# Performance work log

Measured on AMD Instinct MI355X. Metric: run time of the kernel, lower is better.

The kernel has to match this reference:

```python
import jax, jax.numpy as jnp
import numpy as np

B, S, D = 4, 2048, 1024
H = 2 * D          # hidden_dim = 2*n_embd
A = H // 16        # adapt_dim
E = 8              # num_experts
GS = 4             # group_size
G = E // GS        # num_groups
K = 2              # top-k experts within group


def _ln(x, g, b, eps=1e-5):
    m = x.mean(-1, keepdims=True)
    v = ((x - m) ** 2).mean(-1, keepdims=True)
    return (x - m) * jax.lax.rsqrt(v + eps) * g + b


def setup_inputs() -> dict:
    key = jax.random.key(0)
    ks = jax.random.split(key, 14)
    n = lambda k, shape, s: jax.random.normal(k, shape, jnp.float32) * s
    sc = 1.0 / float(np.sqrt(D))
    asc = 0.01 / float(np.sqrt(A))
    return {
        'x': n(ks[0], (B, S, D), 1.0),
        'Wu': n(ks[1], (H, D), sc),        # shared_up
        'Wg': n(ks[2], (H, D), sc),        # shared_gate
        'Wd': n(ks[3], (D, H), sc),        # shared_down
        'Wpre': n(ks[4], (A, D), sc * 0.01),   # pre_adapt
        'Wpost': n(ks[5], (A, H), sc * 0.01),  # post_adapt
        'ln_g': jnp.ones((A,), jnp.float32),
        'ln_b': jnp.zeros((A,), jnp.float32),
        'Wap': n(ks[6], (H, A), sc * 0.01),    # adapt_proj
        'Wea': n(ks[7], (E, A, A), asc),       # per-expert adapter linears
        'ln_eg': jnp.ones((E, A), jnp.float32),
        'ln_eb': jnp.zeros((E, A), jnp.float32),
        'Wep': n(ks[8], (H, A), asc),          # expert_proj
        'Wop': n(ks[9], (D, H), asc),          # output_proj
        'Wgr': n(ks[10], (G, D), 0.001),       # router_group
        'Wer': n(ks[11], (GS, D), 0.001),      # router_expert
    }


def _forward(x, Wu, Wg, Wd, Wpre, Wpost, ln_g, ln_b, Wap, Wea, ln_eg, ln_eb, Wep, Wop, Wgr, Wer):
    N = B * S
    xf = x.reshape(N, D)
    # --- hierarchical router ---
    gl = xf @ Wgr.T                              # [N,G]
    gp = jax.nn.softmax(gl, axis=-1)
    gw, gi = jax.lax.top_k(gp, 1)                # top-1 group
    el = xf @ Wer.T                              # [N,GS]
    ep = jax.nn.softmax(el, axis=-1)
    lw, li = jax.lax.top_k(ep, K)                # top-k local experts
    lw = lw / (lw.sum(-1, keepdims=True) + 1e-7)
    fw = gw * lw                                 # [N,K] final weights
    idx = gi * GS + li                           # [N,K] global expert ids (distinct per token)
    dispatch = jnp.zeros((N, E), x.dtype).at[jnp.arange(N)[:, None], idx].set(fw)
    load = dispatch.sum(0)
    target = load.sum() / E
    rloss = 0.001 * (jnp.mean((load - target) ** 2) + jnp.mean(gl ** 2) + jnp.mean(el ** 2))
    # --- shared expert MLP ---
    hidden = jax.nn.silu(x @ Wg.T) * (x @ Wu.T)  # [B,S,H]
    ai = _ln(x @ Wpre.T, ln_g, ln_b)             # [B,S,A]
    ao = _ln(hidden @ Wpost.T, ln_g, ln_b)       # [B,S,A]
    aw = jax.nn.silu(jnp.clip(jnp.einsum('bsa,bta->bst', ai, ao), -5.0, 5.0))  # [B,S,S]
    adapt = jnp.einsum('bst,bta->bsa', aw, ai) @ Wap.T
    hidden = hidden + 0.1 * adapt
    shared = hidden @ Wd.T                       # [B,S,D]
    # --- expert group (dense form of masked gather/scatter; w==0 off-mask) ---
    w = dispatch.reshape(B, S, E)
    h0 = x @ Wpre.T                              # [B,S,A]
    he = _ln(jnp.einsum('bsa,eca->bsec', h0, Wea), ln_eg, ln_eb)  # [B,S,E,A]
    M = Wop @ Wep                                # output_proj o expert_proj, [D,A]
    out = shared * w.sum(-1, keepdims=True) + 0.1 * jnp.einsum('bsec,bse,dc->bsd', he, w, M)
    return out, rloss


def reference(x, Wu, Wg, Wd, Wpre, Wpost, ln_g, ln_b, Wap, Wea, ln_eg, ln_eb, Wep, Wop, Wgr, Wer):
    return _forward(x, Wu, Wg, Wd, Wpre, Wpost, ln_g, ln_b, Wap, Wea, ln_eg, ln_eb, Wep, Wop, Wgr, Wer)
```

## Files before the change

kernel.cpp:

```cpp
#include <hip/hip_runtime.h>
#include <math.h>


typedef __bf16 bf16_t;
typedef __attribute__((ext_vector_type(8))) __bf16 bf16x8;
typedef __attribute__((ext_vector_type(4))) float f32x4;

__device__ __forceinline__ float b2f(bf16_t v) { return (float)v; }
__device__ __forceinline__ bf16_t f2b(float v) { return (bf16_t)v; }
__device__ __forceinline__ float siluf(float v) { return v / (1.f + expf(-v)); }

static constexpr int Bb = 4, S = 2048, D = 1024, H = 2048, A = 128, E = 8;
static constexpr int N = Bb * S;

typedef __attribute__((address_space(1))) void gvoid;
typedef __attribute__((address_space(3))) void svoid;
__device__ __forceinline__ void gll16(const bf16_t* g, bf16_t* l) {
  __builtin_amdgcn_global_load_lds((gvoid*)g, (svoid*)l, 16, 0, 0);
}

__device__ __forceinline__ long tidx(int row, int k, int K, int lgTR) {
  int TRm = (1 << lgTR) - 1;
  int q = (k >> 3) & 3;
  int p = q ^ ((row >> 1) & 3);
  return ((((long)(row >> lgTR) * (K >> 5) + (k >> 5)) << lgTR) + (row & TRm)) * 32 +
         ((long)p << 3);
}

__device__ __forceinline__ bf16x8 ld8f(const float* p) {
  float4 a = *reinterpret_cast<const float4*>(p);
  float4 b = *reinterpret_cast<const float4*>(p + 4);
  bf16x8 r;
  r[0] = f2b(a.x); r[1] = f2b(a.y); r[2] = f2b(a.z); r[3] = f2b(a.w);
  r[4] = f2b(b.x); r[5] = f2b(b.y); r[6] = f2b(b.z); r[7] = f2b(b.w);
  return r;
}
__device__ __forceinline__ void split8(const float* p, bf16x8& h, bf16x8& l) {
  float4 a = *reinterpret_cast<const float4*>(p);
  float4 b = *reinterpret_cast<const float4*>(p + 4);
  float v[8] = {a.x, a.y, a.z, a.w, b.x, b.y, b.z, b.w};
#pragma unroll
  for (int j = 0; j < 8; j++) {
    bf16_t hh = f2b(v[j]);
    h[j] = hh;
    l[j] = f2b(v[j] - b2f(hh));
  }
}
__device__ __forceinline__ bf16x8 ld8m(const void* p, int row, int k, int K, int m) {
  if (m == 1) return ld8f(reinterpret_cast<const float*>(p) + (long)row * K + k);
  if (m == 2)
    return *reinterpret_cast<const bf16x8*>(
        reinterpret_cast<const bf16_t*>(p) + tidx(row, k, K, 7));
  return *reinterpret_cast<const bf16x8*>(
      reinterpret_cast<const bf16_t*>(p) + (long)row * K + k);
}

template <int LGTR, int LGNKS>
__global__ __launch_bounds__(256) void split_tiled(
    const float* __restrict__ in, bf16_t* __restrict__ hi,
    bf16_t* __restrict__ lo, long total, int K) {
  long stride = (long)gridDim.x * 256;
  for (long o = (long)blockIdx.x * 256 + threadIdx.x; o < total; o += stride) {
    int p = (int)(o & 3);
    long t = o >> 2;
    int r = (int)(t & ((1 << LGTR) - 1));
    long t2 = t >> LGTR;
    int ks = (int)(t2 & ((1 << LGNKS) - 1));
    long rt = t2 >> LGNKS;
    long row = (rt << LGTR) + r;
    int k = (ks << 5) + ((p ^ ((r >> 1) & 3)) << 3);
    bf16x8 h, l;
    split8(in + row * K + k, h, l);
    reinterpret_cast<bf16x8*>(hi)[o] = h;
    reinterpret_cast<bf16x8*>(lo)[o] = l;
  }
}

template <int LGTR, int LGNKS>
__global__ __launch_bounds__(256) void split_tiled2(
    const float* __restrict__ s0, bf16_t* __restrict__ h0, bf16_t* __restrict__ l0,
    const float* __restrict__ s1, bf16_t* __restrict__ h1, bf16_t* __restrict__ l1,
    long total, int K) {
  const float* in = blockIdx.z ? s1 : s0;
  bf16_t* hi = blockIdx.z ? h1 : h0;
  bf16_t* lo = blockIdx.z ? l1 : l0;
  long stride = (long)gridDim.x * 256;
  for (long o = (long)blockIdx.x * 256 + threadIdx.x; o < total; o += stride) {
    int p = (int)(o & 3);
    long t = o >> 2;
    int r = (int)(t & ((1 << LGTR) - 1));
    long t2 = t >> LGTR;
    int ks = (int)(t2 & ((1 << LGNKS) - 1));
    long rt = t2 >> LGNKS;
    long row = (rt << LGTR) + r;
    int k = (ks << 5) + ((p ^ ((r >> 1) & 3)) << 3);
    bf16x8 h, l;
    split8(in + row * K + k, h, l);
    reinterpret_cast<bf16x8*>(hi)[o] = h;
    reinterpret_cast<bf16x8*>(lo)[o] = l;
  }
}

template <int WM, int WN, int MODE>
__global__ __launch_bounds__(256) void gemm_nt_b(
    const void* __restrict__ Ag, const void* __restrict__ Bg,
    void* __restrict__ Cv, int M, int Nn, int K,
    const float* __restrict__ aux, int aF, int bF) {
  constexpr int BM = 2 * WM, BN = 2 * WN, AM = WM / 16, AN = WN / 16;
  constexpr int LDT = 40;
  __shared__ alignas(16) bf16_t As[BM * LDT];
  __shared__ alignas(16) bf16_t Bs[BN * LDT];

  const int tid = threadIdx.x;
  const int wave = tid >> 6, lane = tid & 63;
  const int wr = wave >> 1, wc = wave & 1;
  const int quad = lane >> 4, l16 = lane & 15;
  const int rowA0 = blockIdx.y * BM, rowB0 = blockIdx.x * BN;

  f32x4 acc[AM][AN] = {};

  for (int k0 = 0; k0 < K; k0 += 32) {
    for (int c = tid; c < BM * 4; c += 256) {
      int r = c >> 2, kc = c & 3;
      *reinterpret_cast<bf16x8*>(&As[r * LDT + kc * 8]) =
          ld8m(Ag, rowA0 + r, k0 + kc * 8, K, aF);
    }
    for (int c = tid; c < BN * 4; c += 256) {
      int r = c >> 2, kc = c & 3;
      *reinterpret_cast<bf16x8*>(&Bs[r * LDT + kc * 8]) =
          ld8m(Bg, rowB0 + r, k0 + kc * 8, K, bF);
    }
    __syncthreads();
    bf16x8 af[AM], bfv[AN];
#pragma unroll
    for (int i = 0; i < AM; i++)
      af[i] = *reinterpret_cast<bf16x8*>(&As[(wr * WM + i * 16 + l16) * LDT + quad * 8]);
#pragma unroll
    for (int j = 0; j < AN; j++)
      bfv[j] = *reinterpret_cast<bf16x8*>(&Bs[(wc * WN + j * 16 + l16) * LDT + quad * 8]);
#pragma unroll
    for (int i = 0; i < AM; i++)
#pragma unroll
      for (int j = 0; j < AN; j++)
        acc[i][j] = __builtin_amdgcn_mfma_f32_16x16x32_bf16(af[i], bfv[j], acc[i][j], 0, 0, 0);
    __syncthreads();
  }

#pragma unroll
  for (int i = 0; i < AM; i++)
#pragma unroll
    for (int j = 0; j < AN; j++)
#pragma unroll
      for (int r = 0; r < 4; r++) {
        int row = rowA0 + wr * WM + i * 16 + quad * 4 + r;
        int col = rowB0 + wc * WN + j * 16 + l16;
        long o = (long)row * Nn + col;
        float v = acc[i][j][r];
        if constexpr (MODE == 0) {
          reinterpret_cast<bf16_t*>(Cv)[o] = f2b(v);
        } else if constexpr (MODE == 1) {
          v = fminf(fmaxf(v, -5.f), 5.f);
          reinterpret_cast<bf16_t*>(Cv)[o] = f2b(siluf(v));
        } else if constexpr (MODE == 2) {
          float* C = reinterpret_cast<float*>(Cv);
          C[o] = C[o] + 0.1f * v;
        } else {
          float* C = reinterpret_cast<float*>(Cv);
          C[o] = C[o] * aux[row] + 0.1f * v;
        }
      }
}

__global__ __launch_bounds__(256) void gemm_gu_g(
    const bf16_t* __restrict__ xhT, const bf16_t* __restrict__ xlT,
    const bf16_t* __restrict__ WghT, const bf16_t* __restrict__ WglT,
    const bf16_t* __restrict__ WuhT, const bf16_t* __restrict__ WulT,
    bf16_t* __restrict__ Hh, bf16_t* __restrict__ Hl) {
  __shared__ alignas(16) bf16_t Ah[128 * 32];
  __shared__ alignas(16) bf16_t Al[128 * 32];
  __shared__ alignas(16) bf16_t B1h[64 * 32];
  __shared__ alignas(16) bf16_t B1l[64 * 32];
  __shared__ alignas(16) bf16_t B2h[64 * 32];
  __shared__ alignas(16) bf16_t B2l[64 * 32];

  const int tid = threadIdx.x;
  const int wave = tid >> 6, lane = tid & 63;
  const int wr = wave >> 1, wc = wave & 1;
  const int quad = lane >> 4, l16 = lane & 15;
  const int sw = (quad ^ ((l16 >> 1) & 3)) << 3;
  const int lid = blockIdx.y * gridDim.x + blockIdx.x;
  const int nper = (gridDim.x * gridDim.y) >> 3;
  const int nl = (lid & 7) * nper + (lid >> 3);
  const int bm = nl >> 5, bn = nl & 31;
  constexpr int nks = D / 32;
  const int wo = wave << 9;

  f32x4 ag[4][2] = {}, au[4][2] = {};

  for (int ks = 0; ks < nks; ks++) {
    long ao = (((long)bm * nks + ks) << 12) + wo + lane * 8;
    long bo = (((long)bn * nks + ks) << 11) + wo + lane * 8;
    gll16(xhT + ao, Ah + wo);
    gll16(xhT + ao + 2048, Ah + wo + 2048);
    gll16(xlT + ao, Al + wo);
    gll16(xlT + ao + 2048, Al + wo + 2048);
    gll16(WghT + bo, B1h + wo);
    gll16(WglT + bo, B1l + wo);
    gll16(WuhT + bo, B2h + wo);
    gll16(WulT + bo, B2l + wo);
    __syncthreads();
    bf16x8 afh[4], afl[4], b1h[2], b1l[2], b2h[2], b2l[2];
#pragma unroll
    for (int i = 0; i < 4; i++) {
      int ro = (wr * 64 + i * 16 + l16) * 32 + sw;
      afh[i] = *reinterpret_cast<bf16x8*>(&Ah[ro]);
      afl[i] = *reinterpret_cast<bf16x8*>(&Al[ro]);
    }
#pragma unroll
    for (int j = 0; j < 2; j++) {
      int ro = (wc * 32 + j * 16 + l16) * 32 + sw;
      b1h[j] = *reinterpret_cast<bf16x8*>(&B1h[ro]);
      b1l[j] = *reinterpret_cast<bf16x8*>(&B1l[ro]);
      b2h[j] = *reinterpret_cast<bf16x8*>(&B2h[ro]);
      b2l[j] = *reinterpret_cast<bf16x8*>(&B2l[ro]);
    }
#pragma unroll
    for (int i = 0; i < 4; i++)
#pragma unroll
      for (int j = 0; j < 2; j++) {
        ag[i][j] = __builtin_amdgcn_mfma_f32_16x16x32_bf16(afh[i], b1h[j], ag[i][j], 0, 0, 0);
        ag[i][j] = __builtin_amdgcn_mfma_f32_16x16x32_bf16(afh[i], b1l[j], ag[i][j], 0, 0, 0);
        ag[i][j] = __builtin_amdgcn_mfma_f32_16x16x32_bf16(afl[i], b1h[j], ag[i][j], 0, 0, 0);
        au[i][j] = __builtin_amdgcn_mfma_f32_16x16x32_bf16(afh[i], b2h[j], au[i][j], 0, 0, 0);
        au[i][j] = __builtin_amdgcn_mfma_f32_16x16x32_bf16(afh[i], b2l[j], au[i][j], 0, 0, 0);
        au[i][j] = __builtin_amdgcn_mfma_f32_16x16x32_bf16(afl[i], b2h[j], au[i][j], 0, 0, 0);
      }
    __syncthreads();
  }

#pragma unroll
  for (int i = 0; i < 4; i++)
#pragma unroll
    for (int j = 0; j < 2; j++)
#pragma unroll
      for (int r = 0; r < 4; r++) {
        int row = bm * 128 + wr * 64 + i * 16 + quad * 4 + r;
        int col = bn * 64 + wc * 32 + j * 16 + l16;
        long o = tidx(row, col, H, 7) + (col & 7);
        float v = siluf(ag[i][j][r]) * au[i][j][r];
        bf16_t hh = f2b(v);
        Hh[o] = hh;
        Hl[o] = f2b(v - b2f(hh));
      }
}

__global__ __launch_bounds__(256) void gemm_dn_g(
    const bf16_t* __restrict__ HhT, const bf16_t* __restrict__ HlT,
    const bf16_t* __restrict__ WdhT, const bf16_t* __restrict__ WdlT,
    const bf16_t* __restrict__ hw2, const bf16_t* __restrict__ Mb2,
    const float* __restrict__ wsum, float* __restrict__ Cg) {
  __shared__ alignas(16) bf16_t Ah[128 * 32];
  __shared__ alignas(16) bf16_t Al[128 * 32];
  __shared__ alignas(16) bf16_t Bh[128 * 32];
  __shared__ alignas(16) bf16_t Bl[128 * 32];

  const int tid = threadIdx.x;
  const int wave = tid >> 6, lane = tid & 63;
  const int wr = wave >> 1, wc = wave & 1;
  const int quad = lane >> 4, l16 = lane & 15;
  const int sw = (quad ^ ((l16 >> 1) & 3)) << 3;
  const int lid = blockIdx.y * gridDim.x + blockIdx.x;
  const int nper = (gridDim.x * gridDim.y) >> 3;
  const int nl = (lid & 7) * nper + (lid >> 3);
  const int by = nl >> 3, bx = nl & 7;
  constexpr int nks = H / 32;
  const int wo = wave << 9;

  f32x4 acc[4][4] = {};

  for (int ks = 0; ks < nks; ks++) {
    long ao = (((long)by * nks + ks) << 12) + wo + lane * 8;
    long bo = (((long)bx * nks + ks) << 12) + wo + lane * 8;
    gll16(HhT + ao, Ah + wo);
    gll16(HhT + ao + 2048, Ah + wo + 2048);
    gll16(HlT + ao, Al + wo);
    gll16(HlT + ao + 2048, Al + wo + 2048);
    gll16(WdhT + bo, Bh + wo);
    gll16(WdhT + bo + 2048, Bh + wo + 2048);
    gll16(WdlT + bo, Bl + wo);
    gll16(WdlT + bo + 2048, Bl + wo + 2048);
    __syncthreads();
    bf16x8 afh[4], afl[4], bfh[4], bfl[4];
#pragma unroll
    for (int i = 0; i < 4; i++) {
      int ro = (wr * 64 + i * 16 + l16) * 32 + sw;
      afh[i] = *reinterpret_cast<bf16x8*>(&Ah[ro]);
      afl[i] = *reinterpret_cast<bf16x8*>(&Al[ro]);
    }
#pragma unroll
    for (int j = 0; j < 4; j++) {
      int ro = (wc * 64 + j * 16 + l16) * 32 + sw;
      bfh[j] = *reinterpret_cast<bf16x8*>(&Bh[ro]);
      bfl[j] = *reinterpret_cast<bf16x8*>(&Bl[ro]);
    }
#pragma unroll
    for (int i = 0; i < 4; i++)
#pragma unroll
      for (int j = 0; j < 4; j++) {
        acc[i][j] = __builtin_amdgcn_mfma_f32_16x16x32_bf16(afh[i], bfh[j], acc[i][j], 0, 0, 0);
        acc[i][j] = __builtin_amdgcn_mfma_f32_16x16x32_bf16(afh[i], bfl[j], acc[i][j], 0, 0, 0);
        acc[i][j] = __builtin_amdgcn_mfma_f32_16x16x32_bf16(afl[i], bfh[j], acc[i][j], 0, 0, 0);
      }
    __syncthreads();
  }

  {
    const int rrow = wave * 16 + (lane >> 2);
    const int pp = lane & 3;
    for (int ck = 0; ck < 8; ck++) {
      int r0 = rrow, r1 = rrow + 64;
      int q0 = (pp ^ ((r0 >> 1) & 3)) << 3;
      int q1 = (pp ^ ((r1 >> 1) & 3)) << 3;
      gll16(hw2 + ((long)(by * 128 + r0) * 256 + ck * 32 + q0), Ah + wo);
      gll16(hw2 + ((long)(by * 128 + r1) * 256 + ck * 32 + q1), Ah + wo + 2048);
      gll16(Mb2 + ((long)(bx * 128 + r0) * 256 + ck * 32 + q0), Bh + wo);
      gll16(Mb2 + ((long)(bx * 128 + r1) * 256 + ck * 32 + q1), Bh + wo + 2048);
      __syncthreads();
      bf16x8 af2[4], bf2[4];
#pragma unroll
      for (int i = 0; i < 4; i++)
        af2[i] = *reinterpret_cast<bf16x8*>(&Ah[(wr * 64 + i * 16 + l16) * 32 + sw]);
#pragma unroll
      for (int j = 0; j < 4; j++)
        bf2[j] = *reinterpret_cast<bf16x8*>(&Bh[(wc * 64 + j * 16 + l16) * 32 + sw]);
#pragma unroll
      for (int i = 0; i < 4; i++)
#pragma unroll
        for (int j = 0; j < 4; j++)
          acc[i][j] = __builtin_amdgcn_mfma_f32_16x16x32_bf16(af2[i], bf2[j], acc[i][j], 0, 0, 0);
      __syncthreads();
    }
  }

#pragma unroll
  for (int i = 0; i < 4; i++)
#pragma unroll
    for (int j = 0; j < 4; j++)
#pragma unroll
      for (int r = 0; r < 4; r++) {
        int row = by * 128 + wr * 64 + i * 16 + quad * 4 + r;
        int col = bx * 128 + wc * 64 + j * 16 + l16;
        Cg[(long)row * D + col] = wsum[row] * acc[i][j][r];
      }
}

__global__ __launch_bounds__(256) void fused_adapt(
    const bf16_t* __restrict__ aib, const bf16_t* __restrict__ aob,
    const bf16_t* __restrict__ aiT, bf16_t* __restrict__ outp,
    int oLd, int oOff, float cscale) {
  constexpr int LDQ = 136;
  constexpr int LDP = 72;
  __shared__ alignas(16) bf16_t Qs[64 * LDQ];
  __shared__ alignas(16) bf16_t Os[64 * LDQ];
  __shared__ alignas(16) bf16_t Ps[64 * LDP];
  __shared__ alignas(16) bf16_t Vs[128 * LDP];

  const int tid = threadIdx.x;
  const int wave = tid >> 6, lane = tid & 63;
  const int wr = wave >> 1, wc = wave & 1;
  const int quad = lane >> 4, l16 = lane & 15;
  const int b = blockIdx.y;
  const int q0 = blockIdx.x * 64;

  for (int c = tid; c < 1024; c += 256) {
    int r = c >> 4, cc = c & 15;
    *reinterpret_cast<bf16x8*>(&Qs[r * LDQ + cc * 8]) =
        *reinterpret_cast<const bf16x8*>(&aib[((long)b * S + q0 + r) * A + cc * 8]);
  }

  f32x4 o[2][4] = {};

  for (int tt = 0; tt < S / 64; tt++) {
    const int t0 = tt * 64;
    __syncthreads();
    for (int c = tid; c < 1024; c += 256) {
      int r = c >> 4, cc = c & 15;
      *reinterpret_cast<bf16x8*>(&Os[r * LDQ + cc * 8]) =
          *reinterpret_cast<const bf16x8*>(&aob[((long)b * S + t0 + r) * A + cc * 8]);
    }
    for (int c = tid; c < 1024; c += 256) {
      int r = c >> 3, cc = c & 7;
      *reinterpret_cast<bf16x8*>(&Vs[r * LDP + cc * 8]) =
          *reinterpret_cast<const bf16x8*>(&aiT[((long)b * A + r) * S + t0 + cc * 8]);
    }
    __syncthreads();
    f32x4 p[2][2] = {};
#pragma unroll
    for (int ks = 0; ks < 4; ks++) {
      bf16x8 af[2], bfv[2];
#pragma unroll
      for (int i = 0; i < 2; i++)
        af[i] = *reinterpret_cast<bf16x8*>(&Qs[(wr * 32 + i * 16 + l16) * LDQ + ks * 32 + quad * 8]);
#pragma unroll
      for (int j = 0; j < 2; j++)
        bfv[j] = *reinterpret_cast<bf16x8*>(&Os[(wc * 32 + j * 16 + l16) * LDQ + ks * 32 + quad * 8]);
#pragma unroll
      for (int i = 0; i < 2; i++)
#pragma unroll
        for (int j = 0; j < 2; j++)
          p[i][j] = __builtin_amdgcn_mfma_f32_16x16x32_bf16(af[i], bfv[j], p[i][j], 0, 0, 0);
    }
#pragma unroll
    for (int i = 0; i < 2; i++)
#pragma unroll
      for (int j = 0; j < 2; j++)
#pragma unroll
        for (int r = 0; r < 4; r++) {
          int row = wr * 32 + i * 16 + quad * 4 + r;
          int col = wc * 32 + j * 16 + l16;
          float v = fminf(fmaxf(p[i][j][r], -5.f), 5.f);
          Ps[row * LDP + col] = f2b(siluf(v));
        }
    __syncthreads();
#pragma unroll
    for (int ks = 0; ks < 2; ks++) {
      bf16x8 paf[2], vbf[4];
#pragma unroll
      for (int i = 0; i < 2; i++)
        paf[i] = *reinterpret_cast<bf16x8*>(&Ps[(wr * 32 + i * 16 + l16) * LDP + ks * 32 + quad * 8]);
#pragma unroll
      for (int j = 0; j < 4; j++)
        vbf[j] = *reinterpret_cast<bf16x8*>(&Vs[(wc * 64 + j * 16 + l16) * LDP + ks * 32 + quad * 8]);
#pragma unroll
      for (int i = 0; i < 2; i++)
#pragma unroll
        for (int j = 0; j < 4; j++)
          o[i][j] = __builtin_amdgcn_mfma_f32_16x16x32_bf16(paf[i], vbf[j], o[i][j], 0, 0, 0);
    }
  }

#pragma unroll
  for (int i = 0; i < 2; i++)
#pragma unroll
    for (int j = 0; j < 4; j++)
#pragma unroll
      for (int r = 0; r < 4; r++) {
        int row = q0 + wr * 32 + i * 16 + quad * 4 + r;
        int col = wc * 64 + j * 16 + l16;
        long token = (long)b * S + row;
        outp[token * oLd + oOff + col] = f2b(o[i][j][r] * cscale);
      }
}

__global__ __launch_bounds__(256) void gemm_mb_splitk(
    const float* __restrict__ Ag, const bf16_t* __restrict__ Bg,
    float* __restrict__ Mp, int M, int Nn, int K) {
  constexpr int BM = 64, BN = 64, LDT = 40;
  __shared__ alignas(16) bf16_t As[BM * LDT];
  __shared__ alignas(16) bf16_t Bs[BN * LDT];
  const int tid = threadIdx.x;
  const int wave = tid >> 6, lane = tid & 63;
  const int wr = wave >> 1, wc = wave & 1;
  const int quad = lane >> 4, l16 = lane & 15;
  const int rowA0 = blockIdx.y * BM, rowB0 = blockIdx.x * BN;
  const int kz = blockIdx.z;
  const int ks0 = kz * (K / 8), ks1 = ks0 + K / 8;

  f32x4 acc[2][2] = {};
  for (int k0 = ks0; k0 < ks1; k0 += 32) {
    for (int c = tid; c < BM * 4; c += 256) {
      int r = c >> 2, kc = c & 3;
      *reinterpret_cast<bf16x8*>(&As[r * LDT + kc * 8]) =
          ld8f(Ag + (long)(rowA0 + r) * K + k0 + kc * 8);
    }
    for (int c = tid; c < BN * 4; c += 256) {
      int r = c >> 2, kc = c & 3;
      *reinterpret_cast<bf16x8*>(&Bs[r * LDT + kc * 8]) =
          *reinterpret_cast<const bf16x8*>(&Bg[(long)(rowB0 + r) * K + k0 + kc * 8]);
    }
    __syncthreads();
    bf16x8 af[2], bfv[2];
#pragma unroll
    for (int i = 0; i < 2; i++)
      af[i] = *reinterpret_cast<bf16x8*>(&As[(wr * 32 + i * 16 + l16) * LDT + quad * 8]);
#pragma unroll
    for (int j = 0; j < 2; j++)
      bfv[j] = *reinterpret_cast<bf16x8*>(&Bs[(wc * 32 + j * 16 + l16) * LDT + quad * 8]);
#pragma unroll
    for (int i = 0; i < 2; i++)
#pragma unroll
      for (int j = 0; j < 2; j++)
        acc[i][j] = __builtin_amdgcn_mfma_f32_16x16x32_bf16(af[i], bfv[j], acc[i][j], 0, 0, 0);
    __syncthreads();
  }
#pragma unroll
  for (int i = 0; i < 2; i++)
#pragma unroll
    for (int j = 0; j < 2; j++)
#pragma unroll
      for (int r = 0; r < 4; r++) {
        int row = rowA0 + wr * 32 + i * 16 + quad * 4 + r;
        int col = rowB0 + wc * 32 + j * 16 + l16;
        Mp[(long)kz * M * Nn + (long)row * Nn + col] = acc[i][j][r];
      }
}

__global__ __launch_bounds__(256) void mb_combine(
    const float* __restrict__ Mp, bf16_t* __restrict__ outp, int total,
    int ld, int coff) {
  int i = blockIdx.x * 256 + threadIdx.x;
  if (i >= total) return;
  float s = 0.f;
#pragma unroll
  for (int z = 0; z < 8; z++) s += Mp[(long)z * total + i];
  outp[(long)(i >> 7) * ld + coff + (i & 127)] = f2b(s);
}

__global__ __launch_bounds__(256) void gemm_dn_hl(
    const float* __restrict__ Ag, const float* __restrict__ Bg,
    float* __restrict__ Cg, int M, int Nn, int K) {
  constexpr int BM = 128, BN = 128, LDT = 40;
  __shared__ alignas(16) bf16_t Ah[BM * LDT];
  __shared__ alignas(16) bf16_t Al[BM * LDT];
  __shared__ alignas(16) bf16_t Bh[BN * LDT];
  __shared__ alignas(16) bf16_t Bl[BN * LDT];

  const int tid = threadIdx.x;
  const int wave = tid >> 6, lane = tid & 63;
  const int wr = wave >> 1, wc = wave & 1;
  const int quad = lane >> 4, l16 = lane & 15;
  const int rowA0 = blockIdx.y * BM, rowB0 = blockIdx.x * BN;

  f32x4 acc[4][4] = {};

  for (int k0 = 0; k0 < K; k0 += 32) {
    for (int c = tid; c < BM * 4; c += 256) {
      int r = c >> 2, kc = c & 3;
      bf16x8 h, l;
      split8(&Ag[(long)(rowA0 + r) * K + k0 + kc * 8], h, l);
      *reinterpret_cast<bf16x8*>(&Ah[r * LDT + kc * 8]) = h;
      *reinterpret_cast<bf16x8*>(&Al[r * LDT + kc * 8]) = l;
    }
    for (int c = tid; c < BN * 4; c += 256) {
      int r = c >> 2, kc = c & 3;
      bf16x8 h, l;
      split8(&Bg[(long)(rowB0 + r) * K + k0 + kc * 8], h, l);
      *reinterpret_cast<bf16x8*>(&Bh[r * LDT + kc * 8]) = h;
      *reinterpret_cast<bf16x8*>(&Bl[r * LDT + kc * 8]) = l;
    }
    __syncthreads();
    bf16x8 afh[4], afl[4], bfh[4], bfl[4];
#pragma unroll
    for (int i = 0; i < 4; i++) {
      int ro = (wr * 64 + i * 16 + l16) * LDT + quad * 8;
      afh[i] = *reinterpret_cast<bf16x8*>(&Ah[ro]);
      afl[i] = *reinterpret_cast<bf16x8*>(&Al[ro]);
    }
#pragma unroll
    for (int j = 0; j < 4; j++) {
      int ro = (wc * 64 + j * 16 + l16) * LDT + quad * 8;
      bfh[j] = *reinterpret_cast<bf16x8*>(&Bh[ro]);
      bfl[j] = *reinterpret_cast<bf16x8*>(&Bl[ro]);
    }
#pragma unroll
    for (int i = 0; i < 4; i++)
#pragma unroll
      for (int j = 0; j < 4; j++) {
        acc[i][j] = __builtin_amdgcn_mfma_f32_16x16x32_bf16(afh[i], bfh[j], acc[i][j], 0, 0, 0);
        acc[i][j] = __builtin_amdgcn_mfma_f32_16x16x32_bf16(afh[i], bfl[j], acc[i][j], 0, 0, 0);
        acc[i][j] = __builtin_amdgcn_mfma_f32_16x16x32_bf16(afl[i], bfh[j], acc[i][j], 0, 0, 0);
      }
    __syncthreads();
  }

#pragma unroll
  for (int i = 0; i < 4; i++)
#pragma unroll
    for (int j = 0; j < 4; j++)
#pragma unroll
      for (int r = 0; r < 4; r++) {
        int row = rowA0 + wr * 64 + i * 16 + quad * 4 + r;
        int col = rowB0 + wc * 64 + j * 16 + l16;
        Cg[(long)row * Nn + col] = acc[i][j][r];
      }
}

__global__ __launch_bounds__(256) void gemm_gu_hl(
    const float* __restrict__ x, const float* __restrict__ Wg,
    const float* __restrict__ Wu, float* __restrict__ Cg, int M, int Nn, int K) {
  constexpr int BM = 128, BN = 64, LDT = 40;
  __shared__ alignas(16) bf16_t Ah[BM * LDT];
  __shared__ alignas(16) bf16_t Al[BM * LDT];
  __shared__ alignas(16) bf16_t B1h[BN * LDT];
  __shared__ alignas(16) bf16_t B1l[BN * LDT];
  __shared__ alignas(16) bf16_t B2h[BN * LDT];
  __shared__ alignas(16) bf16_t B2l[BN * LDT];

  const int tid = threadIdx.x;
  const int wave = tid >> 6, lane = tid & 63;
  const int wr = wave >> 1, wc = wave & 1;
  const int quad = lane >> 4, l16 = lane & 15;
  const int rowA0 = blockIdx.y * BM, rowB0 = blockIdx.x * BN;

  f32x4 ag[4][2] = {}, au[4][2] = {};

  for (int k0 = 0; k0 < K; k0 += 32) {
    for (int c = tid; c < BM * 4; c += 256) {
      int r = c >> 2, kc = c & 3;
      bf16x8 h, l;
      split8(&x[(long)(rowA0 + r) * K + k0 + kc * 8], h, l);
      *reinterpret_cast<bf16x8*>(&Ah[r * LDT + kc * 8]) = h;
      *reinterpret_cast<bf16x8*>(&Al[r * LDT + kc * 8]) = l;
    }
    for (int c = tid; c < BN * 4; c += 256) {
      int r = c >> 2, kc = c & 3;
      long idx = (long)(rowB0 + r) * K + k0 + kc * 8;
      bf16x8 h, l;
      split8(&Wg[idx], h, l);
      *reinterpret_cast<bf16x8*>(&B1h[r * LDT + kc * 8]) = h;
      *reinterpret_cast<bf16x8*>(&B1l[r * LDT + kc * 8]) = l;
      split8(&Wu[idx], h, l);
      *reinterpret_cast<bf16x8*>(&B2h[r * LDT + kc * 8]) = h;
      *reinterpret_cast<bf16x8*>(&B2l[r * LDT + kc * 8]) = l;
    }
    __syncthreads();
    bf16x8 afh[4], afl[4], b1h[2], b1l[2], b2h[2], b2l[2];
#pragma unroll
    for (int i = 0; i < 4; i++) {
      int ro = (wr * 64 + i * 16 + l16) * LDT + quad * 8;
      afh[i] = *reinterpret_cast<bf16x8*>(&Ah[ro]);
      afl[i] = *reinterpret_cast<bf16x8*>(&Al[ro]);
    }
#pragma unroll
    for (int j = 0; j < 2; j++) {
      int ro = (wc * 32 + j * 16 + l16) * LDT + quad * 8;
      b1h[j] = *reinterpret_cast<bf16x8*>(&B1h[ro]);
      b1l[j] = *reinterpret_cast<bf16x8*>(&B1l[ro]);
      b2h[j] = *reinterpret_cast<bf16x8*>(&B2h[ro]);
      b2l[j] = *reinterpret_cast<bf16x8*>(&B2l[ro]);
    }
#pragma unroll
    for (int i = 0; i < 4; i++)
#pragma unroll
      for (int j = 0; j < 2; j++) {
        ag[i][j] = __builtin_amdgcn_mfma_f32_16x16x32_bf16(afh[i], b1h[j], ag[i][j], 0, 0, 0);
        ag[i][j] = __builtin_amdgcn_mfma_f32_16x16x32_bf16(afh[i], b1l[j], ag[i][j], 0, 0, 0);
        ag[i][j] = __builtin_amdgcn_mfma_f32_16x16x32_bf16(afl[i], b1h[j], ag[i][j], 0, 0, 0);
        au[i][j] = __builtin_amdgcn_mfma_f32_16x16x32_bf16(afh[i], b2h[j], au[i][j], 0, 0, 0);
        au[i][j] = __builtin_amdgcn_mfma_f32_16x16x32_bf16(afh[i], b2l[j], au[i][j], 0, 0, 0);
        au[i][j] = __builtin_amdgcn_mfma_f32_16x16x32_bf16(afl[i], b2h[j], au[i][j], 0, 0, 0);
      }
    __syncthreads();
  }

#pragma unroll
  for (int i = 0; i < 4; i++)
#pragma unroll
    for (int j = 0; j < 2; j++)
#pragma unroll
      for (int r = 0; r < 4; r++) {
        int row = rowA0 + wr * 64 + i * 16 + quad * 4 + r;
        int col = rowB0 + wc * 32 + j * 16 + l16;
        Cg[(long)row * Nn + col] = siluf(ag[i][j][r]) * au[i][j][r];
      }
}

__global__ __launch_bounds__(256) void router_kernel(
    const float* __restrict__ x, const float* __restrict__ Wgr,
    const float* __restrict__ Wer, int* __restrict__ eidx,
    float* __restrict__ fw, float* __restrict__ wsum,
    float* __restrict__ lpart) {
  __shared__ float part[4][12];
  const int wv = threadIdx.x >> 6;
  const int lane = threadIdx.x & 63;
  const int token = blockIdx.x * 4 + wv;
  if (lane < 12) part[wv][lane] = 0.f;
  const float* xp = x + (long)token * D;
  float xr[16];
#pragma unroll
  for (int i = 0; i < 16; i++) xr[i] = xp[lane + i * 64];
  float dots[6];
#pragma unroll
  for (int w = 0; w < 6; w++) {
    const float* wp = (w < 2) ? (Wgr + (long)w * D) : (Wer + (long)(w - 2) * D);
    float s = 0.f;
#pragma unroll
    for (int i = 0; i < 16; i++) s += xr[i] * wp[lane + i * 64];
#pragma unroll
    for (int off = 32; off; off >>= 1) s += __shfl_xor(s, off);
    dots[w] = s;
  }
  if (lane == 0) {
    float gl0 = dots[0], gl1 = dots[1];
    float mg = fmaxf(gl0, gl1);
    float e0 = expf(gl0 - mg), e1 = expf(gl1 - mg);
    float inv = 1.f / (e0 + e1);
    float gp0 = e0 * inv, gp1 = e1 * inv;
    int gi = (gp1 > gp0) ? 1 : 0;
    float gw = gi ? gp1 : gp0;
    float el[4] = {dots[2], dots[3], dots[4], dots[5]};
    float me = fmaxf(fmaxf(el[0], el[1]), fmaxf(el[2], el[3]));
    float ep[4], es = 0.f;
#pragma unroll
    for (int j = 0; j < 4; j++) { ep[j] = expf(el[j] - me); es += ep[j]; }
    float inve = 1.f / es;
#pragma unroll
    for (int j = 0; j < 4; j++) ep[j] *= inve;
    int i1 = 0;
    for (int j = 1; j < 4; j++) if (ep[j] > ep[i1]) i1 = j;
    int i2 = (i1 == 0) ? 1 : 0;
    for (int j = 0; j < 4; j++) if (j != i1 && j != i2 && ep[j] > ep[i2]) i2 = j;
    float l1 = ep[i1], l2 = ep[i2];
    float ils = 1.f / (l1 + l2 + 1e-7f);
    float f1 = gw * l1 * ils, f2 = gw * l2 * ils;
    eidx[token * 2] = gi * 4 + i1;
    eidx[token * 2 + 1] = gi * 4 + i2;
    fw[token * 2] = f1;
    fw[token * 2 + 1] = f2;
    wsum[token] = f1 + f2;
    part[wv][gi * 4 + i1] = f1;
    part[wv][gi * 4 + i2] = f2;
    part[wv][8] = gl0 * gl0 + gl1 * gl1;
    part[wv][9] = el[0] * el[0] + el[1] * el[1] + el[2] * el[2] + el[3] * el[3];
  }
  __syncthreads();
  if (threadIdx.x < 12) {
    lpart[(long)blockIdx.x * 12 + threadIdx.x] =
        part[0][threadIdx.x] + part[1][threadIdx.x] +
        part[2][threadIdx.x] + part[3][threadIdx.x];
  }
}

__global__ __launch_bounds__(256) void ln_rows(
    const bf16_t* __restrict__ in, const float* __restrict__ g,
    const float* __restrict__ b, bf16_t* __restrict__ out) {
  const int row = blockIdx.x * 4 + (threadIdx.x >> 6);
  const int lane = threadIdx.x & 63;
  const bf16_t* p = in + (long)row * A;
  float x0 = b2f(p[lane]), x1 = b2f(p[lane + 64]);
  float s = x0 + x1;
#pragma unroll
  for (int off = 32; off; off >>= 1) s += __shfl_xor(s, off);
  float mean = s * (1.f / 128.f);
  float d0 = x0 - mean, d1 = x1 - mean;
  float q = d0 * d0 + d1 * d1;
#pragma unroll
  for (int off = 32; off; off >>= 1) q += __shfl_xor(q, off);
  float r = rsqrtf(q * (1.f / 128.f) + 1e-5f);
  bf16_t* po = out + (long)row * A;
  po[lane] = f2b(d0 * r * g[lane] + b[lane]);
  po[lane + 64] = f2b(d1 * r * g[lane + 64] + b[lane + 64]);
}

__global__ __launch_bounds__(256) void transpose2d(
    const void* __restrict__ in, bf16_t* __restrict__ out, int R, int C, int isf) {
  __shared__ bf16_t t[32][33];
  const long zb = blockIdx.z;
  const long ib = zb * (long)R * C;
  bf16_t* op = out + zb * (long)R * C;
  const int r0 = blockIdx.y * 32, c0 = blockIdx.x * 32;
  const int tx = threadIdx.x & 31, ty = threadIdx.x >> 5;
#pragma unroll
  for (int i = 0; i < 4; i++) {
    long idx = ib + (long)(r0 + ty + i * 8) * C + c0 + tx;
    t[ty + i * 8][tx] = isf ? f2b(reinterpret_cast<const float*>(in)[idx])
                            : reinterpret_cast<const bf16_t*>(in)[idx];
  }
  __syncthreads();
#pragma unroll
  for (int i = 0; i < 4; i++) op[(long)(c0 + ty + i * 8) * R + r0 + tx] = t[tx][ty + i * 8];
}

__global__ __launch_bounds__(128) void expert_adapt(
    const bf16_t* __restrict__ h0, const bf16_t* __restrict__ WeaT,
    const float* __restrict__ ln_eg, const float* __restrict__ ln_eb,
    const int* __restrict__ eidx, const float* __restrict__ fw,
    bf16_t* __restrict__ hw, int ld, const float* __restrict__ wsc) {
  const int n = blockIdx.x;
  const int c = threadIdx.x;
  __shared__ float h0s[128];
  __shared__ float red[4];
  h0s[c] = b2f(h0[(long)n * A + c]);
  __syncthreads();
  float out = 0.f;
  for (int k = 0; k < 2; k++) {
    int e = eidx[n * 2 + k];
    e = min(max(e, 0), E - 1);
    float w = fw[n * 2 + k];
    const bf16_t* Wc = WeaT + (long)e * A * A + c;
    float t = 0.f;
#pragma unroll 8
    for (int a = 0; a < 128; a++) t += b2f(Wc[(long)a * A]) * h0s[a];
    float s = t, q = t * t;
#pragma unroll
    for (int off = 32; off; off >>= 1) { s += __shfl_xor(s, off); q += __shfl_xor(q, off); }
    if ((c & 63) == 0) { red[(c >> 6) * 2] = s; red[(c >> 6) * 2 + 1] = q; }
    __syncthreads();
    float Sx = red[0] + red[2], Qx = red[1] + red[3];
    float mean = Sx * (1.f / 128.f);
    float var = Qx * (1.f / 128.f) - mean * mean;
    float r = rsqrtf(var + 1e-5f);
    out += w * ((t - mean) * r * ln_eg[e * A + c] + ln_eb[e * A + c]);
    __syncthreads();
  }
  float sc = wsc ? (0.1f / wsc[n]) : 1.f;
  hw[(long)n * ld + c] = f2b(out * sc);
}

__global__ __launch_bounds__(256) void finalize_loss(
    const float* __restrict__ lpart, int nblk, float* __restrict__ outv) {
  float acc[10] = {};
  for (int b = threadIdx.x; b < nblk; b += 256) {
    const float* p = lpart + (long)b * 12;
#pragma unroll
    for (int c = 0; c < 10; c++) acc[c] += p[c];
  }
  __shared__ float red[10][4];
  const int lane = threadIdx.x & 63, wv = threadIdx.x >> 6;
#pragma unroll
  for (int c = 0; c < 10; c++) {
    float s = acc[c];
#pragma unroll
    for (int off = 32; off; off >>= 1) s += __shfl_xor(s, off);
    if (lane == 0) red[c][wv] = s;
  }
  __syncthreads();
  if (threadIdx.x == 0) {
    float loss[10];
#pragma unroll
    for (int c = 0; c < 10; c++)
      loss[c] = red[c][0] + red[c][1] + red[c][2] + red[c][3];
    float tl = 0.f;
    for (int e = 0; e < 8; e++) tl += loss[e];
    float target = tl / 8.f;
    float mse = 0.f;
    for (int e = 0; e < 8; e++) { float d = loss[e] - target; mse += d * d; }
    mse *= (1.f / 8.f);
    outv[0] = 0.001f * (mse + loss[8] / (float)(N * 2) + loss[9] / (float)(N * 4));
  }
}

extern "C" void kernel_launch(void* const* d_in, const int* in_sizes, int n_in,
                              void* d_out, int out_size, void* d_ws, size_t ws_size,
                              hipStream_t stream) {
  const float* x = (const float*)d_in[0];
  const float* Wu = (const float*)d_in[1];
  const float* Wg = (const float*)d_in[2];
  const float* Wd = (const float*)d_in[3];
  const float* Wpre = (const float*)d_in[4];
  const float* Wpost = (const float*)d_in[5];
  const float* ln_g = (const float*)d_in[6];
  const float* ln_b = (const float*)d_in[7];
  const float* Wap = (const float*)d_in[8];
  const float* Wea = (const float*)d_in[9];
  const float* ln_eg = (const float*)d_in[10];
  const float* ln_eb = (const float*)d_in[11];
  const float* Wep = (const float*)d_in[12];
  const float* Wop = (const float*)d_in[13];
  const float* Wgr = (const float*)d_in[14];
  const float* Wer = (const float*)d_in[15];
  float* out = (float*)d_out;

  char* ws = (char*)d_ws;
  size_t off = 0;
  auto alloc = [&](size_t bytes) { char* p = ws + off; off += (bytes + 255) & ~size_t(255); return p; };
  float* lpart = (float*)alloc((size_t)(N / 4) * 12 * 4);
  float* wsum = (float*)alloc((size_t)N * 4);
  float* fwb = (float*)alloc((size_t)N * 2 * 4);
  int* eidx = (int*)alloc((size_t)N * 2 * 4);
  bf16_t* Mb2 = (bf16_t*)alloc((size_t)D * 256 * 2);
  float* Mp = (float*)alloc((size_t)8 * D * A * 4);
  bf16_t* WepT = (bf16_t*)alloc((size_t)H * A * 2);
  bf16_t* WapT = (bf16_t*)alloc((size_t)H * A * 2);
  bf16_t* hw2 = (bf16_t*)alloc((size_t)N * 256 * 2);
  bf16_t* h0b = (bf16_t*)alloc((size_t)N * A * 2);
  bf16_t* aib = (bf16_t*)alloc((size_t)N * A * 2);
  bf16_t* scrA = (bf16_t*)alloc((size_t)N * A * 2);
  bf16_t* aob = (bf16_t*)alloc((size_t)N * A * 2);
  bf16_t* WeaT = (bf16_t*)alloc((size_t)E * A * A * 2);
  bf16_t* aopre = scrA;
  bf16_t* aiT = scrA;

  const bool big = ws_size >= ((size_t)140 << 20);
  float* hiddenF = nullptr;
  bf16_t *xh = nullptr, *xl = nullptr;
  bf16_t *Wgh = nullptr, *Wgl = nullptr, *Wuh = nullptr, *Wul = nullptr;
  bf16_t *Wdh = nullptr, *Wdl = nullptr, *Hh = nullptr, *Hl = nullptr;
  if (big) {
    xh = (bf16_t*)alloc((size_t)N * D * 2);
    xl = (bf16_t*)alloc((size_t)N * D * 2);
    Wgh = (bf16_t*)alloc((size_t)H * D * 2);
    Wgl = (bf16_t*)alloc((size_t)H * D * 2);
    Wuh = (bf16_t*)alloc((size_t)H * D * 2);
    Wul = (bf16_t*)alloc((size_t)H * D * 2);
    Wdh = (bf16_t*)alloc((size_t)D * H * 2);
    Wdl = (bf16_t*)alloc((size_t)D * H * 2);
    Hh = (bf16_t*)alloc((size_t)N * H * 2);
    Hl = (bf16_t*)alloc((size_t)N * H * 2);
  } else {
    hiddenF = (float*)alloc((size_t)N * H * 4);
  }
  (void)ws_size; (void)in_sizes; (void)n_in; (void)out_size;

  const dim3 blk(256);

  router_kernel<<<dim3(N / 4), blk, 0, stream>>>(x, Wgr, Wer, eidx, fwb, wsum, lpart);
  transpose2d<<<dim3(A / 32, A / 32, E), blk, 0, stream>>>(Wea, WeaT, A, A, 1);

  if (big) {
    split_tiled<7, 5><<<dim3(2048), blk, 0, stream>>>(x, xh, xl, (long)N * D / 8, D);
    split_tiled2<6, 5><<<dim3(512, 1, 2), blk, 0, stream>>>(
        Wg, Wgh, Wgl, Wu, Wuh, Wul, (long)H * D / 8, D);
    split_tiled<7, 6><<<dim3(512), blk, 0, stream>>>(Wd, Wdh, Wdl, (long)D * H / 8, H);
    gemm_gu_g<<<dim3(H / 64, N / 128), blk, 0, stream>>>(
        xh, xl, Wgh, Wgl, Wuh, Wul, Hh, Hl);
    gemm_nt_b<16, 32, 0><<<dim3(A / 64, N / 32), blk, 0, stream>>>(
        xh, Wpre, h0b, N, A, D, nullptr, 2, 1);
    ln_rows<<<dim3(N / 4), blk, 0, stream>>>(h0b, ln_g, ln_b, aib);
    gemm_nt_b<16, 32, 0><<<dim3(A / 64, N / 32), blk, 0, stream>>>(
        Hh, Wpost, aopre, N, A, H, nullptr, 2, 1);
    ln_rows<<<dim3(N / 4), blk, 0, stream>>>(aopre, ln_g, ln_b, aob);
    transpose2d<<<dim3(A / 32, S / 32, Bb), blk, 0, stream>>>(aib, aiT, S, A, 0);
    transpose2d<<<dim3(A / 32, H / 32, 1), blk, 0, stream>>>(Wep, WepT, H, A, 1);
    transpose2d<<<dim3(A / 32, H / 32, 1), blk, 0, stream>>>(Wap, WapT, H, A, 1);
    gemm_mb_splitk<<<dim3(A / 64, D / 64, 8), blk, 0, stream>>>(Wop, WepT, Mp, D, A, H);
    mb_combine<<<dim3((D * A + 255) / 256), blk, 0, stream>>>(Mp, Mb2, D * A, 256, 0);
    gemm_mb_splitk<<<dim3(A / 64, D / 64, 8), blk, 0, stream>>>(Wd, WapT, Mp, D, A, H);
    mb_combine<<<dim3((D * A + 255) / 256), blk, 0, stream>>>(Mp, Mb2, D * A, 256, 128);
    fused_adapt<<<dim3(S / 64, Bb), blk, 0, stream>>>(
        aib, aob, aiT, hw2, 256, 128, 0.1f);
    expert_adapt<<<dim3(N), dim3(128), 0, stream>>>(
        h0b, WeaT, ln_eg, ln_eb, eidx, fwb, hw2, 256, wsum);
    gemm_dn_g<<<dim3(D / 128, N / 128), blk, 0, stream>>>(
        Hh, Hl, Wdh, Wdl, hw2, Mb2, wsum, out);
  } else {
    bf16_t* adpreb = hw2 + (size_t)N * A;
    gemm_gu_hl<<<dim3(H / 64, N / 128), blk, 0, stream>>>(x, Wg, Wu, hiddenF, N, H, D);
    gemm_nt_b<16, 32, 0><<<dim3(A / 64, N / 32), blk, 0, stream>>>(
        x, Wpre, h0b, N, A, D, nullptr, 1, 1);
    ln_rows<<<dim3(N / 4), blk, 0, stream>>>(h0b, ln_g, ln_b, aib);
    gemm_nt_b<16, 32, 0><<<dim3(A / 64, N / 32), blk, 0, stream>>>(
        hiddenF, Wpost, aopre, N, A, H, nullptr, 1, 1);
    ln_rows<<<dim3(N / 4), blk, 0, stream>>>(aopre, ln_g, ln_b, aob);
    transpose2d<<<dim3(A / 32, S / 32, Bb), blk, 0, stream>>>(aib, aiT, S, A, 0);
    fused_adapt<<<dim3(S / 64, Bb), blk, 0, stream>>>(
        aib, aob, aiT, adpreb, 128, 0, 1.f);
    gemm_nt_b<64, 64, 2><<<dim3(H / 128, N / 128), blk, 0, stream>>>(
        adpreb, Wap, hiddenF, N, H, A, nullptr, 0, 1);
    gemm_dn_hl<<<dim3(D / 128, N / 128), blk, 0, stream>>>(hiddenF, Wd, out, N, D, H);
    transpose2d<<<dim3(A / 32, H / 32, 1), blk, 0, stream>>>(Wep, WepT, H, A, 1);
    gemm_mb_splitk<<<dim3(A / 64, D / 64, 8), blk, 0, stream>>>(Wop, WepT, Mp, D, A, H);
    mb_combine<<<dim3((D * A + 255) / 256), blk, 0, stream>>>(Mp, Mb2, D * A, 128, 0);
    expert_adapt<<<dim3(N), dim3(128), 0, stream>>>(
        h0b, WeaT, ln_eg, ln_eb, eidx, fwb, hw2, 128, nullptr);
    gemm_nt_b<64, 64, 3><<<dim3(D / 128, N / 128), blk, 0, stream>>>(
        hw2, Mb2, out, N, D, A, wsum, 0, 0);
  }

  finalize_loss<<<dim3(1), blk, 0, stream>>>(lpart, N / 4, out + (size_t)N * D);
}
```

Before: 731.5 us.

## Halve fused_adapt query tile, pre-convert adapter weights, merge weight transposes

fused_adapt now processes 32 query rows per block instead of 64, doubling the grid from 128 to 256 blocks so the device's compute units are better filled. Each block reloads the O/V tiles for fewer rows, so total load traffic goes up. Wpre and Wpost are converted to bf16 once by a new kernel, so the GEMMs no longer convert fp32 weights on the fly. The two weight transposes are merged into one launch.

```diff
diff --git a/kernel.cpp b/kernel.cpp
--- a/kernel.cpp
+++ b/kernel.cpp
@@ -101,6 +101,17 @@
   }
 }
 
+__global__ __launch_bounds__(256) void cvt_bf16_2(
+    const float* __restrict__ s0, bf16_t* __restrict__ d0, long n0,
+    const float* __restrict__ s1, bf16_t* __restrict__ d1, long n1) {
+  long total = n0 + n1;
+  long stride = (long)gridDim.x * 256;
+  for (long i = (long)blockIdx.x * 256 + threadIdx.x; i < total; i += stride) {
+    if (i < n0) reinterpret_cast<bf16x8*>(d0)[i] = ld8f(s0 + i * 8);
+    else reinterpret_cast<bf16x8*>(d1)[i - n0] = ld8f(s1 + (i - n0) * 8);
+  }
+}
+
 template <int WM, int WN, int MODE>
 __global__ __launch_bounds__(256) void gemm_nt_b(
     const void* __restrict__ Ag, const void* __restrict__ Bg,
@@ -360,9 +371,9 @@
     int oLd, int oOff, float cscale) {
   constexpr int LDQ = 136;
   constexpr int LDP = 72;
-  __shared__ alignas(16) bf16_t Qs[64 * LDQ];
+  __shared__ alignas(16) bf16_t Qs[32 * LDQ];
   __shared__ alignas(16) bf16_t Os[64 * LDQ];
-  __shared__ alignas(16) bf16_t Ps[64 * LDP];
+  __shared__ alignas(16) bf16_t Ps[32 * LDP];
   __shared__ alignas(16) bf16_t Vs[128 * LDP];
 
   const int tid = threadIdx.x;
@@ -370,15 +381,15 @@
   const int wr = wave >> 1, wc = wave & 1;
   const int quad = lane >> 4, l16 = lane & 15;
   const int b = blockIdx.y;
-  const int q0 = blockIdx.x * 64;
-
-  for (int c = tid; c < 1024; c += 256) {
+  const int q0 = blockIdx.x * 32;
+
+  for (int c = tid; c < 512; c += 256) {
     int r = c >> 4, cc = c & 15;
     *reinterpret_cast<bf16x8*>(&Qs[r * LDQ + cc * 8]) =
         *reinterpret_cast<const bf16x8*>(&aib[((long)b * S + q0 + r) * A + cc * 8]);
   }
 
-  f32x4 o[2][4] = {};
+  f32x4 o[4] = {};
 
   for (int tt = 0; tt < S / 64; tt++) {
     const int t0 = tt * 64;
@@ -394,62 +405,52 @@
           *reinterpret_cast<const bf16x8*>(&aiT[((long)b * A + r) * S + t0 + cc * 8]);
     }
     __syncthreads();
-    f32x4 p[2][2] = {};
+    f32x4 p[2] = {};
 #pragma unroll
     for (int ks = 0; ks < 4; ks++) {
-      bf16x8 af[2], bfv[2];
-#pragma unroll
-      for (int i = 0; i < 2; i++)
-        af[i] = *reinterpret_cast<bf16x8*>(&Qs[(wr * 32 + i * 16 + l16) * LDQ + ks * 32 + quad * 8]);
+      bf16x8 af =
+          *reinterpret_cast<bf16x8*>(&Qs[(wr * 16 + l16) * LDQ + ks * 32 + quad * 8]);
+      bf16x8 bfv[2];
 #pragma unroll
       for (int j = 0; j < 2; j++)
         bfv[j] = *reinterpret_cast<bf16x8*>(&Os[(wc * 32 + j * 16 + l16) * LDQ + ks * 32 + quad * 8]);
 #pragma unroll
-      for (int i = 0; i < 2; i++)
-#pragma unroll
-        for (int j = 0; j < 2; j++)
-          p[i][j] = __builtin_amdgcn_mfma_f32_16x16x32_bf16(af[i], bfv[j], p[i][j], 0, 0, 0);
-    }
-#pragma unroll
-    for (int i = 0; i < 2; i++)
-#pragma unroll
       for (int j = 0; j < 2; j++)
-#pragma unroll
-        for (int r = 0; r < 4; r++) {
-          int row = wr * 32 + i * 16 + quad * 4 + r;
-          int col = wc * 32 + j * 16 + l16;
-          float v = fminf(fmaxf(p[i][j][r], -5.f), 5.f);
-          Ps[row * LDP + col] = f2b(siluf(v));
-        }
+        p[j] = __builtin_amdgcn_mfma_f32_16x16x32_bf16(af, bfv[j], p[j], 0, 0, 0);
+    }
+#pragma unroll
+    for (int j = 0; j < 2; j++)
+#pragma unroll
+      for (int r = 0; r < 4; r++) {
+        int row = wr * 16 + quad * 4 + r;
+        int col = wc * 32 + j * 16 + l16;
+        float v = fminf(fmaxf(p[j][r], -5.f), 5.f);
+        Ps[row * LDP + col] = f2b(siluf(v));
+      }
     __syncthreads();
 #pragma unroll
     for (int ks = 0; ks < 2; ks++) {
-      bf16x8 paf[2], vbf[4];
-#pragma unroll
-      for (int i = 0; i < 2; i++)
-        paf[i] = *reinterpret_cast<bf16x8*>(&Ps[(wr * 32 + i * 16 + l16) * LDP + ks * 32 + quad * 8]);
+      bf16x8 paf =
+          *reinterpret_cast<bf16x8*>(&Ps[(wr * 16 + l16) * LDP + ks * 32 + quad * 8]);
+      bf16x8 vbf[4];
 #pragma unroll
       for (int j = 0; j < 4; j++)
         vbf[j] = *reinterpret_cast<bf16x8*>(&Vs[(wc * 64 + j * 16 + l16) * LDP + ks * 32 + quad * 8]);
 #pragma unroll
-      for (int i = 0; i < 2; i++)
-#pragma unroll
-        for (int j = 0; j < 4; j++)
-          o[i][j] = __builtin_amdgcn_mfma_f32_16x16x32_bf16(paf[i], vbf[j], o[i][j], 0, 0, 0);
-    }
-  }
-
-#pragma unroll
-  for (int i = 0; i < 2; i++)
-#pragma unroll
-    for (int j = 0; j < 4; j++)
-#pragma unroll
-      for (int r = 0; r < 4; r++) {
-        int row = q0 + wr * 32 + i * 16 + quad * 4 + r;
-        int col = wc * 64 + j * 16 + l16;
-        long token = (long)b * S + row;
-        outp[token * oLd + oOff + col] = f2b(o[i][j][r] * cscale);
-      }
+      for (int j = 0; j < 4; j++)
+        o[j] = __builtin_amdgcn_mfma_f32_16x16x32_bf16(paf, vbf[j], o[j], 0, 0, 0);
+    }
+  }
+
+#pragma unroll
+  for (int j = 0; j < 4; j++)
+#pragma unroll
+    for (int r = 0; r < 4; r++) {
+      int row = q0 + wr * 16 + quad * 4 + r;
+      int col = wc * 64 + j * 16 + l16;
+      long token = (long)b * S + row;
+      outp[token * oLd + oOff + col] = f2b(o[j][r] * cscale);
+    }
 }
 
 __global__ __launch_bounds__(256) void gemm_mb_splitk(
@@ -765,6 +766,24 @@
     long idx = ib + (long)(r0 + ty + i * 8) * C + c0 + tx;
     t[ty + i * 8][tx] = isf ? f2b(reinterpret_cast<const float*>(in)[idx])
                             : reinterpret_cast<const bf16_t*>(in)[idx];
+  }
+  __syncthreads();
+#pragma unroll
+  for (int i = 0; i < 4; i++) op[(long)(c0 + ty + i * 8) * R + r0 + tx] = t[tx][ty + i * 8];
+}
+
+__global__ __launch_bounds__(256) void transpose2d_pair(
+    const float* __restrict__ in0, bf16_t* __restrict__ out0,
+    const float* __restrict__ in1, bf16_t* __restrict__ out1, int R, int C) {
+  __shared__ bf16_t t[32][33];
+  const float* in = blockIdx.z ? in1 : in0;
+  bf16_t* op = blockIdx.z ? out1 : out0;
+  const int r0 = blockIdx.y * 32, c0 = blockIdx.x * 32;
+  const int tx = threadIdx.x & 31, ty = threadIdx.x >> 5;
+#pragma unroll
+  for (int i = 0; i < 4; i++) {
+    long idx = (long)(r0 + ty + i * 8) * C + c0 + tx;
+    t[ty + i * 8][tx] = f2b(in[idx]);
   }
   __syncthreads();
 #pragma unroll
@@ -872,6 +891,8 @@
   float* Mp = (float*)alloc((size_t)8 * D * A * 4);
   bf16_t* WepT = (bf16_t*)alloc((size_t)H * A * 2);
   bf16_t* WapT = (bf16_t*)alloc((size_t)H * A * 2);
+  bf16_t* Wpre_b = (bf16_t*)alloc((size_t)A * D * 2);
+  bf16_t* Wpost_b = (bf16_t*)alloc((size_t)A * H * 2);
   bf16_t* hw2 = (bf16_t*)alloc((size_t)N * 256 * 2);
   bf16_t* h0b = (bf16_t*)alloc((size_t)N * A * 2);
   bf16_t* aib = (bf16_t*)alloc((size_t)N * A * 2);
@@ -912,22 +933,24 @@
     split_tiled2<6, 5><<<dim3(512, 1, 2), blk, 0, stream>>>(
         Wg, Wgh, Wgl, Wu, Wuh, Wul, (long)H * D / 8, D);
     split_tiled<7, 6><<<dim3(512), blk, 0, stream>>>(Wd, Wdh, Wdl, (long)D * H / 8, H);
+    cvt_bf16_2<<<dim3(192), blk, 0, stream>>>(
+        Wpre, Wpre_b, (long)A * D / 8, Wpost, Wpost_b, (long)A * H / 8);
     gemm_gu_g<<<dim3(H / 64, N / 128), blk, 0, stream>>>(
         xh, xl, Wgh, Wgl, Wuh, Wul, Hh, Hl);
     gemm_nt_b<16, 32, 0><<<dim3(A / 64, N / 32), blk, 0, stream>>>(
-        xh, Wpre, h0b, N, A, D, nullptr, 2, 1);
+        xh, Wpre_b, h0b, N, A, D, nullptr, 2, 0);
     ln_rows<<<dim3(N / 4), blk, 0, stream>>>(h0b, ln_g, ln_b, aib);
     gemm_nt_b<16, 32, 0><<<dim3(A / 64, N / 32), blk, 0, stream>>>(
-        Hh, Wpost, aopre, N, A, H, nullptr, 2, 1);
+        Hh, Wpost_b, aopre, N, A, H, nullptr, 2, 0);
     ln_rows<<<dim3(N / 4), blk, 0, stream>>>(aopre, ln_g, ln_b, aob);
     transpose2d<<<dim3(A / 32, S / 32, Bb), blk, 0, stream>>>(aib, aiT, S, A, 0);
-    transpose2d<<<dim3(A / 32, H / 32, 1), blk, 0, stream>>>(Wep, WepT, H, A, 1);
-    transpose2d<<<dim3(A / 32, H / 32, 1), blk, 0, stream>>>(Wap, WapT, H, A, 1);
+    transpose2d_pair<<<dim3(A / 32, H / 32, 2), blk, 0, stream>>>(
+        Wep, WepT, Wap, WapT, H, A);
     gemm_mb_splitk<<<dim3(A / 64, D / 64, 8), blk, 0, stream>>>(Wop, WepT, Mp, D, A, H);
     mb_combine<<<dim3((D * A + 255) / 256), blk, 0, stream>>>(Mp, Mb2, D * A, 256, 0);
     gemm_mb_splitk<<<dim3(A / 64, D / 64, 8), blk, 0, stream>>>(Wd, WapT, Mp, D, A, H);
     mb_combine<<<dim3((D * A + 255) / 256), blk, 0, stream>>>(Mp, Mb2, D * A, 256, 128);
-    fused_adapt<<<dim3(S / 64, Bb), blk, 0, stream>>>(
+    fused_adapt<<<dim3(S / 32, Bb), blk, 0, stream>>>(
         aib, aob, aiT, hw2, 256, 128, 0.1f);
     expert_adapt<<<dim3(N), dim3(128), 0, stream>>>(
         h0b, WeaT, ln_eg, ln_eb, eidx, fwb, hw2, 256, wsum);
@@ -943,7 +966,7 @@
         hiddenF, Wpost, aopre, N, A, H, nullptr, 1, 1);
     ln_rows<<<dim3(N / 4), blk, 0, stream>>>(aopre, ln_g, ln_b, aob);
     transpose2d<<<dim3(A / 32, S / 32, Bb), blk, 0, stream>>>(aib, aiT, S, A, 0);
-    fused_adapt<<<dim3(S / 64, Bb), blk, 0, stream>>>(
+    fused_adapt<<<dim3(S / 32, Bb), blk, 0, stream>>>(
         aib, aob, aiT, adpreb, 128, 0, 1.f);
     gemm_nt_b<64, 64, 2><<<dim3(H / 128, N / 128), blk, 0, stream>>>(
         adpreb, Wap, hiddenF, N, H, A, nullptr, 0, 1);
```

New measurement: 679.0 us. 1.08x faster.
